# Kernel optimization log

Measured on AMD Instinct MI355X. Metric: run time of the kernel, lower is better.

## Reference

```python
import jax, jax.numpy as jnp
import numpy as np

D_MODEL = 1024
D_INTERNAL = 1024
B, T = 4, 2048
ROPE_BASE = 10000.0


def _rotate_half(x):
    h = x.shape[-1] // 2
    return jnp.concatenate([-x[..., h:], x[..., :h]], axis=-1)


def _justnorm(x):
    return x / jnp.linalg.norm(x, axis=-1, keepdims=True)


def setup_inputs() -> dict:
    key = jax.random.key(0)
    k1, k2 = jax.random.split(key)
    stdev = 1.0 / (D_MODEL + D_INTERNAL) ** 0.5
    qkv_w = jax.random.uniform(k1, (3 * D_INTERNAL, D_MODEL), minval=-stdev, maxval=stdev, dtype=jnp.float32)
    qkv_w = _justnorm(qkv_w)  # source normalizes qkv rows at init
    sqk = (D_MODEL ** -0.5) * jnp.ones((D_INTERNAL,), dtype=jnp.float32)  # sqk_init_scaling * ones
    input_vecs = jax.random.normal(k2, (B, T, D_MODEL), dtype=jnp.float32)
    return {"input_vecs": input_vecs, "qkv_w": qkv_w, "sqk": sqk}


def reference(input_vecs, qkv_w, sqk):
    d_model = input_vecs.shape[-1]
    d_int = qkv_w.shape[0] // 3
    t_len = input_vecs.shape[-2]

    # QKV projection: F.linear(x, W) == x @ W.T
    qkv = jnp.einsum('btc,dc->btd', input_vecs, qkv_w)
    Q, K, V = jnp.split(qkv, 3, axis=-1)  # each [B, T, d_int]

    # Rotary embeddings over full d_int
    inv_freq = 1.0 / (ROPE_BASE ** (jnp.arange(0, d_int, 2, dtype=jnp.float32) / d_int))
    t = jnp.arange(t_len, dtype=jnp.float32)
    freqs = t[:, None] * inv_freq[None, :]              # [T, d_int/2]
    emb = jnp.concatenate([freqs, freqs], axis=-1)      # [T, d_int]
    cos, sin = jnp.cos(emb), jnp.sin(emb)
    Q = Q * cos + _rotate_half(Q) * sin
    K = K * cos + _rotate_half(K) * sin

    # L2 QK-norm with learned per-channel scale (sqk * (1.0 / sqk_init_scaling))
    sqk_eff = sqk * (d_model ** 0.5)
    Q = _justnorm(Q) * sqk_eff
    K = _justnorm(K) * sqk_eff

    # SDPA, eval path: causal, dropout=0, scale = C ** 0.5
    scale = d_model ** 0.5
    scores = jnp.einsum('bqd,bkd->bqk', Q, K) * scale   # [B, T, T]
    causal = jnp.tril(jnp.ones((t_len, t_len), dtype=bool))
    scores = jnp.where(causal[None, :, :], scores, -jnp.inf)
    attn = jax.nn.softmax(scores, axis=-1)
    out = jnp.einsum('bqk,bkd->bqd', attn, V)
    return out
```

## Files before the change

### kernel.cpp

```cpp
#include <hip/hip_runtime.h>

typedef unsigned short u16;
typedef short s16x8 __attribute__((ext_vector_type(8)));
typedef float f32x4 __attribute__((ext_vector_type(4)));

__device__ __forceinline__ u16 f2bf(float f) {
    union { float f; unsigned u; } v; v.f = f;
    unsigned r = v.u + 0x7FFFu + ((v.u >> 16) & 1u);
    return (u16)(r >> 16);
}
__device__ __forceinline__ float bf2f(u16 h) {
    union { unsigned u; float f; } v; v.u = ((unsigned)h) << 16;
    return v.f;
}
__device__ __forceinline__ u16 f2h(float f) {
    _Float16 h = (_Float16)f;
    union { _Float16 h; u16 u; } v; v.h = h; return v.u;
}
__device__ __forceinline__ float h2f(u16 u) {
    union { u16 u; _Float16 h; } v; v.u = u; return (float)v.h;
}

__device__ __forceinline__ void gl_lds16(const u16* g, u16* l) {
    __builtin_amdgcn_global_load_lds(
        (const __attribute__((address_space(1))) void*)g,
        (__attribute__((address_space(3))) void*)l,
        16, 0, 0);
}

__global__ __launch_bounds__(256) void f32_to_bf16(const float* __restrict__ in,
                                                   u16* __restrict__ out, int n) {
    int i = (blockIdx.x * 256 + threadIdx.x) * 4;
    int stride = gridDim.x * 256 * 4;
    for (; i < n; i += stride) {
        float4 v = *reinterpret_cast<const float4*>(in + i);
        ushort4 o;
        o.x = f2bf(v.x); o.y = f2bf(v.y); o.z = f2bf(v.z); o.w = f2bf(v.w);
        *reinterpret_cast<ushort4*>(out + i) = o;
    }
}

template <typename CT>
__device__ __forceinline__ void store_c(CT* p, float v) {
    if constexpr (__is_same(CT, u16))            *p = f2bf(v);
    else if constexpr (__is_same(CT, _Float16))  *p = (_Float16)v;
    else                                         *p = v;
}

__device__ __forceinline__ s16x8 ldfrag(const u16* base, int row, int kk, int fq) {
    int cb = ((kk << 6) + (fq << 4)) ^ ((row & 7) << 4);
    return *reinterpret_cast<const s16x8*>(base + row * 64 + (cb >> 1));
}

template <int MODE, typename CT>
__global__ __launch_bounds__(512)
void gemm_bt(const u16* __restrict__ A, const u16* __restrict__ B, CT* __restrict__ C,
             int K, int lda, int ldb, int ldc, long sA, long sB, long sC) {
    int bx = blockIdx.x, by = blockIdx.y, bz = blockIdx.z;
    if (MODE == 0) {
        int bid = blockIdx.x;
        int xcd = bid & 7, idx = bid >> 3;
        int r = idx >> 6, w = idx & 63;
        bx = r * 8 + (w & 7);
        by = xcd * 8 + (w >> 3);
        bz = 0;
    }
    if (MODE == 1 && bx > by) return;
    if (MODE == 2) { bz = blockIdx.y & 3; by = 15 - (int)(blockIdx.y >> 2); }
    A += (size_t)bz * sA; B += (size_t)bz * sB; C += (size_t)bz * sC;
    int kend = K;
    if (MODE == 2) { int kl = (by + 1) * 128; kend = kl < K ? kl : K; }
    const int NT = kend >> 6;

    __shared__ u16 lds[32768];

    const int tid  = threadIdx.x;
    const int lane = tid & 63;
    const int wave = tid >> 6;
    const int wr = (wave >> 2) * 64;
    const int wc = (wave & 3) * 32;
    const int fr = lane & 15;
    const int fq = lane >> 4;
    const int tm = by * 128, tn = bx * 128;

    const int srow = tid >> 3;
    const int gco  = (((tid & 7) ^ (srow & 7)) << 3);
    const u16* aR[2]; const u16* bR[2];
#pragma unroll
    for (int j = 0; j < 2; ++j) {
        aR[j] = A + (size_t)(tm + j * 64 + srow) * lda + gco;
        bR[j] = B + (size_t)(tn + j * 64 + srow) * ldb + gco;
    }

#define STAGE(b2, k0) do {                                                        \
    _Pragma("unroll") for (int j = 0; j < 2; ++j)                                 \
        gl_lds16(aR[j] + (k0), lds + (b2) * 16384 + j * 4096 + wave * 512);       \
    _Pragma("unroll") for (int j = 0; j < 2; ++j)                                 \
        gl_lds16(bR[j] + (k0), lds + (b2) * 16384 + 8192 + j * 4096 + wave * 512);\
  } while (0)

    f32x4 acc[4][2];
#pragma unroll
    for (int m = 0; m < 4; ++m)
#pragma unroll
        for (int n = 0; n < 2; ++n) acc[m][n] = {0.f, 0.f, 0.f, 0.f};

    STAGE(0, 0);
    if (NT > 1) STAGE(1, 64);

    for (int t = 0; t < NT; ++t) {
        const int buf = t & 1;
        if (t + 1 < NT) { asm volatile("s_waitcnt vmcnt(4)" ::: "memory"); }
        else            { asm volatile("s_waitcnt vmcnt(0)" ::: "memory"); }
        __builtin_amdgcn_s_barrier();
        __builtin_amdgcn_sched_barrier(0);

        const u16* Ab = lds + buf * 16384;
        const u16* Bb = Ab + 8192;
        s16x8 bf0[2], bf1[2];
#pragma unroll
        for (int n = 0; n < 2; ++n) {
            bf0[n] = ldfrag(Bb, wc + n * 16 + fr, 0, fq);
            bf1[n] = ldfrag(Bb, wc + n * 16 + fr, 1, fq);
        }
        __builtin_amdgcn_s_setprio(1);
#pragma unroll
        for (int m = 0; m < 4; ++m) {
            s16x8 a0 = ldfrag(Ab, wr + m * 16 + fr, 0, fq);
            s16x8 a1 = ldfrag(Ab, wr + m * 16 + fr, 1, fq);
#pragma unroll
            for (int n = 0; n < 2; ++n) {
                acc[m][n] = __builtin_amdgcn_mfma_f32_16x16x32_bf16(a0, bf0[n], acc[m][n], 0, 0, 0);
                acc[m][n] = __builtin_amdgcn_mfma_f32_16x16x32_bf16(a1, bf1[n], acc[m][n], 0, 0, 0);
            }
        }
        __builtin_amdgcn_s_setprio(0);
        __builtin_amdgcn_sched_barrier(0);
        __builtin_amdgcn_s_barrier();
        if (t + 2 < NT) STAGE(buf, (t + 2) << 6);
    }
#undef STAGE

#pragma unroll
    for (int m = 0; m < 4; ++m)
#pragma unroll
        for (int n = 0; n < 2; ++n)
#pragma unroll
            for (int r = 0; r < 4; ++r) {
                int row = tm + wr + m * 16 + fq * 4 + r;
                int col = tn + wc + n * 16 + fr;
                store_c(&C[(size_t)row * ldc + col], acc[m][n][r]);
            }
}

__global__ __launch_bounds__(256)
void trig_table(u16* __restrict__ trig) {
    const int t = blockIdx.x;
    const float L = 0.025952563241307517f;
    u16* row = trig + (size_t)t * 1024;
#pragma unroll
    for (int i = 0; i < 2; ++i) {
        int d = threadIdx.x + i * 256;
        float invf = exp2f(-(float)d * L);
        float ang = (float)t * invf;
        float s, c;
        sincosf(ang, &s, &c);
        row[d] = f2h(c);
        row[512 + d] = f2h(s);
    }
}

__global__ __launch_bounds__(256)
void rope_norm(u16* __restrict__ qkv, const float* __restrict__ sqk,
               const u16* __restrict__ trig) {
    const int row = blockIdx.x;
    const int t = row & 2047;
    u16* qp = qkv + (size_t)row * 3072;
    u16* kp = qp + 1024;
    const u16* tb = trig + (size_t)t * 1024;
    const int d = threadIdx.x << 1;

    union U2 { uint u; u16 h[2]; };
    U2 qc0, qc1, kc0, kc1, cc, ss;
    qc0.u = *reinterpret_cast<const uint*>(qp + d);
    qc1.u = *reinterpret_cast<const uint*>(qp + 512 + d);
    kc0.u = *reinterpret_cast<const uint*>(kp + d);
    kc1.u = *reinterpret_cast<const uint*>(kp + 512 + d);
    cc.u  = *reinterpret_cast<const uint*>(tb + d);
    ss.u  = *reinterpret_cast<const uint*>(tb + 512 + d);

    float nq0[2], nq1[2], nk0[2], nk1[2];
    float ssq_q = 0.f, ssq_k = 0.f;
#pragma unroll
    for (int j = 0; j < 2; ++j) {
        float c = h2f(cc.h[j]), s = h2f(ss.h[j]);
        float q0 = bf2f(qc0.h[j]), q1 = bf2f(qc1.h[j]);
        float k0 = bf2f(kc0.h[j]), k1 = bf2f(kc1.h[j]);
        nq0[j] = q0 * c - q1 * s;
        nq1[j] = q1 * c + q0 * s;
        nk0[j] = k0 * c - k1 * s;
        nk1[j] = k1 * c + k0 * s;
        ssq_q += nq0[j] * nq0[j] + nq1[j] * nq1[j];
        ssq_k += nk0[j] * nk0[j] + nk1[j] * nk1[j];
    }

#pragma unroll
    for (int off = 32; off; off >>= 1) {
        ssq_q += __shfl_xor(ssq_q, off);
        ssq_k += __shfl_xor(ssq_k, off);
    }
    __shared__ float red[8];
    int wave = threadIdx.x >> 6, lane = threadIdx.x & 63;
    if (lane == 0) { red[wave] = ssq_q; red[4 + wave] = ssq_k; }
    __syncthreads();
    float rq = rsqrtf(red[0] + red[1] + red[2] + red[3]);
    float rk = rsqrtf(red[4] + red[5] + red[6] + red[7]);

    float2 sq0 = *reinterpret_cast<const float2*>(sqk + d);
    float2 sq1 = *reinterpret_cast<const float2*>(sqk + 512 + d);
    float s0[2] = {sq0.x * 32.f, sq0.y * 32.f};
    float s1[2] = {sq1.x * 32.f, sq1.y * 32.f};

    U2 oq0, oq1, ok0, ok1;
#pragma unroll
    for (int j = 0; j < 2; ++j) {
        oq0.h[j] = f2bf(nq0[j] * rq * s0[j]);
        oq1.h[j] = f2bf(nq1[j] * rq * s1[j]);
        ok0.h[j] = f2bf(nk0[j] * rk * s0[j]);
        ok1.h[j] = f2bf(nk1[j] * rk * s1[j]);
    }
    *reinterpret_cast<uint*>(qp + d)       = oq0.u;
    *reinterpret_cast<uint*>(qp + 512 + d) = oq1.u;
    *reinterpret_cast<uint*>(kp + d)       = ok0.u;
    *reinterpret_cast<uint*>(kp + 512 + d) = ok1.u;
}

__global__ __launch_bounds__(256)
void transpose_v(const u16* __restrict__ qkv, u16* __restrict__ VT) {
    __shared__ u16 tile[32][33];
    int b = blockIdx.z;
    int n0 = blockIdx.x * 32;
    int k0 = blockIdx.y * 32;
    int tx = threadIdx.x, ty = threadIdx.y;
    const u16* src = qkv + (size_t)b * 2048 * 3072 + 2048;
#pragma unroll
    for (int i = 0; i < 4; ++i)
        tile[ty + i * 8][tx] = src[(size_t)(k0 + ty + i * 8) * 3072 + n0 + tx];
    __syncthreads();
    u16* dst = VT + (size_t)b * 1024 * 2048;
#pragma unroll
    for (int i = 0; i < 4; ++i)
        dst[(size_t)(n0 + ty + i * 8) * 2048 + k0 + tx] = tile[tx][ty + i * 8];
}

__global__ __launch_bounds__(256)
void softmax_inplace(u16* __restrict__ Sbase) {
    const int r = blockIdx.x;
    const int b = blockIdx.y;
    u16* row = Sbase + (size_t)b * 4194304 + (size_t)r * 2048;
    const int n = r + 1;
    const int kcap = ((r >> 7) + 1) << 7;
    const int tid = threadIdx.x;
    const bool act = (tid * 8) < kcap;

    union { uint4 u; u16 h[8]; } U;
    if (act) U.u = *reinterpret_cast<const uint4*>(row + tid * 8);
    float v[8];
    float m = -1e30f;
#pragma unroll
    for (int i = 0; i < 8; ++i) {
        int c = tid * 8 + i;
        v[i] = (act && c < n) ? h2f(U.h[i]) : -1e30f;
        m = fmaxf(m, v[i]);
    }
#pragma unroll
    for (int off = 32; off; off >>= 1) m = fmaxf(m, __shfl_xor(m, off));
    __shared__ float redm[4], redsum[4];
    int wave = tid >> 6, lane = tid & 63;
    if (lane == 0) redm[wave] = m;
    __syncthreads();
    m = fmaxf(fmaxf(redm[0], redm[1]), fmaxf(redm[2], redm[3]));
    float M = 32.f * m;

    float sum = 0.f;
#pragma unroll
    for (int i = 0; i < 8; ++i) {
        int c = tid * 8 + i;
        float e = (v[i] > -1e29f) ? __expf(32.f * v[i] - M) : 0.f;
        if (c >= n) e = 0.f;
        v[i] = e;
        sum += e;
    }
#pragma unroll
    for (int off = 32; off; off >>= 1) sum += __shfl_xor(sum, off);
    if (lane == 0) redsum[wave] = sum;
    __syncthreads();
    sum = redsum[0] + redsum[1] + redsum[2] + redsum[3];
    float inv = 1.f / sum;

    if (act) {
        union { uint4 u; u16 h[8]; } O;
#pragma unroll
        for (int i = 0; i < 8; ++i) O.h[i] = f2bf(v[i] * inv);
        *reinterpret_cast<uint4*>(row + tid * 8) = O.u;
    }
}

extern "C" void kernel_launch(void* const* d_in, const int* in_sizes, int n_in,
                              void* d_out, int out_size, void* d_ws, size_t ws_size,
                              hipStream_t stream) {
    const float* x   = (const float*)d_in[0];
    const float* w   = (const float*)d_in[1];
    const float* sqk = (const float*)d_in[2];
    float* out = (float*)d_out;

    const size_t SZ_XB  = (size_t)8192 * 1024 * 2;
    const size_t SZ_WB  = (size_t)3072 * 1024 * 2;
    const size_t SZ_QKV = (size_t)8192 * 3072 * 2;
    const size_t SZ_S   = (size_t)4 * 2048 * 2048 * 2;
    const size_t SZ_TR  = (size_t)2048 * 1024 * 2;
    if (ws_size < SZ_XB + SZ_WB + SZ_QKV + SZ_S + SZ_TR) return;

    char* ws = (char*)d_ws;
    u16* xb   = (u16*)ws;  ws += SZ_XB;
    u16* wb   = (u16*)ws;  ws += SZ_WB;
    u16* qkv  = (u16*)ws;  ws += SZ_QKV;
    u16* S    = (u16*)ws;  ws += SZ_S;
    u16* trig = (u16*)ws;
    u16* VT   = xb;

    f32_to_bf16<<<2048, 256, 0, stream>>>(x, xb, 8192 * 1024);
    f32_to_bf16<<<768, 256, 0, stream>>>(w, wb, 3072 * 1024);

    gemm_bt<0, u16><<<dim3(1536, 1, 1), 512, 0, stream>>>(
        xb, wb, qkv, 1024, 1024, 1024, 3072, 0, 0, 0);

    trig_table<<<2048, 256, 0, stream>>>(trig);
    rope_norm<<<8192, 256, 0, stream>>>(qkv, sqk, trig);

    transpose_v<<<dim3(32, 64, 4), dim3(32, 8), 0, stream>>>(qkv, VT);

    gemm_bt<1, _Float16><<<dim3(16, 16, 4), 512, 0, stream>>>(
        qkv, qkv + 1024, (_Float16*)S, 1024, 3072, 3072, 2048,
        (long)2048 * 3072, (long)2048 * 3072, (long)2048 * 2048);

    softmax_inplace<<<dim3(2048, 4), 256, 0, stream>>>(S);

    gemm_bt<2, float><<<dim3(8, 64, 1), 512, 0, stream>>>(
        S, VT, out, 2048, 2048, 2048, 1024,
        (long)2048 * 2048, (long)1024 * 2048, (long)2048 * 1024);
}
```

Baseline: 167.4 us.

## Enlarge GEMM tiles to 256 rows and fuse V transpose into QKV GEMM epilogue

```diff
diff --git a/kernel.cpp b/kernel.cpp
--- a/kernel.cpp
+++ b/kernel.cpp
@@ -52,84 +52,94 @@
     return *reinterpret_cast<const s16x8*>(base + row * 64 + (cb >> 1));
 }
 
-template <int MODE, typename CT>
-__global__ __launch_bounds__(512)
+template <int MODE, int BNT, typename CT>
+__global__ __launch_bounds__(512, 2)
 void gemm_bt(const u16* __restrict__ A, const u16* __restrict__ B, CT* __restrict__ C,
+             u16* __restrict__ VT,
              int K, int lda, int ldb, int ldc, long sA, long sB, long sC) {
-    int bx = blockIdx.x, by = blockIdx.y, bz = blockIdx.z;
+    constexpr int NF = BNT / 64;
+    constexpr int SB = 16384 + BNT * 64;
+
+    int bx, by, bz;
     if (MODE == 0) {
         int bid = blockIdx.x;
         int xcd = bid & 7, idx = bid >> 3;
-        int r = idx >> 6, w = idx & 63;
-        bx = r * 8 + (w & 7);
-        by = xcd * 8 + (w >> 3);
+        bx = idx % 12;
+        by = xcd * 4 + idx / 12;
         bz = 0;
+    } else {
+        bx = blockIdx.x; by = blockIdx.y; bz = blockIdx.z;
     }
     if (MODE == 1 && bx > by) return;
-    if (MODE == 2) { bz = blockIdx.y & 3; by = 15 - (int)(blockIdx.y >> 2); }
+    if (MODE == 2) by = 7 - by;
     A += (size_t)bz * sA; B += (size_t)bz * sB; C += (size_t)bz * sC;
     int kend = K;
-    if (MODE == 2) { int kl = (by + 1) * 128; kend = kl < K ? kl : K; }
+    if (MODE == 2) { int kl = (by + 1) * 256; kend = kl < K ? kl : K; }
     const int NT = kend >> 6;
 
-    __shared__ u16 lds[32768];
+    __shared__ u16 lds[2 * SB];
 
     const int tid  = threadIdx.x;
     const int lane = tid & 63;
     const int wave = tid >> 6;
-    const int wr = (wave >> 2) * 64;
-    const int wc = (wave & 3) * 32;
+    const int wr = (wave >> 2) * 128;
+    const int wc = (wave & 3) * (BNT / 4);
     const int fr = lane & 15;
     const int fq = lane >> 4;
-    const int tm = by * 128, tn = bx * 128;
+    const int tm = by * 256, tn = bx * BNT;
 
     const int srow = tid >> 3;
     const int gco  = (((tid & 7) ^ (srow & 7)) << 3);
-    const u16* aR[2]; const u16* bR[2];
-#pragma unroll
-    for (int j = 0; j < 2; ++j) {
+    const u16* aR[4]; const u16* bR[NF];
+#pragma unroll
+    for (int j = 0; j < 4; ++j)
         aR[j] = A + (size_t)(tm + j * 64 + srow) * lda + gco;
+#pragma unroll
+    for (int j = 0; j < NF; ++j)
         bR[j] = B + (size_t)(tn + j * 64 + srow) * ldb + gco;
-    }
 
 #define STAGE(b2, k0) do {                                                        \
-    _Pragma("unroll") for (int j = 0; j < 2; ++j)                                 \
-        gl_lds16(aR[j] + (k0), lds + (b2) * 16384 + j * 4096 + wave * 512);       \
-    _Pragma("unroll") for (int j = 0; j < 2; ++j)                                 \
-        gl_lds16(bR[j] + (k0), lds + (b2) * 16384 + 8192 + j * 4096 + wave * 512);\
+    _Pragma("unroll") for (int j = 0; j < 4; ++j)                                 \
+        gl_lds16(aR[j] + (k0), lds + (b2) * SB + j * 4096 + wave * 512);          \
+    _Pragma("unroll") for (int j = 0; j < NF; ++j)                                \
+        gl_lds16(bR[j] + (k0), lds + (b2) * SB + 16384 + j * 4096 + wave * 512);  \
   } while (0)
 
-    f32x4 acc[4][2];
-#pragma unroll
-    for (int m = 0; m < 4; ++m)
-#pragma unroll
-        for (int n = 0; n < 2; ++n) acc[m][n] = {0.f, 0.f, 0.f, 0.f};
+    f32x4 acc[8][NF];
+#pragma unroll
+    for (int m = 0; m < 8; ++m)
+#pragma unroll
+        for (int n = 0; n < NF; ++n) acc[m][n] = {0.f, 0.f, 0.f, 0.f};
 
     STAGE(0, 0);
     if (NT > 1) STAGE(1, 64);
 
     for (int t = 0; t < NT; ++t) {
         const int buf = t & 1;
-        if (t + 1 < NT) { asm volatile("s_waitcnt vmcnt(4)" ::: "memory"); }
-        else            { asm volatile("s_waitcnt vmcnt(0)" ::: "memory"); }
+        if (t + 1 < NT) {
+            if constexpr (NF == 4) asm volatile("s_waitcnt vmcnt(8)" ::: "memory");
+            else                   asm volatile("s_waitcnt vmcnt(6)" ::: "memory");
+        } else {
+            asm volatile("s_waitcnt vmcnt(0)" ::: "memory");
+        }
         __builtin_amdgcn_s_barrier();
         __builtin_amdgcn_sched_barrier(0);
 
-        const u16* Ab = lds + buf * 16384;
-        const u16* Bb = Ab + 8192;
-        s16x8 bf0[2], bf1[2];
-#pragma unroll
-        for (int n = 0; n < 2; ++n) {
+        const u16* Ab = lds + buf * SB;
+        const u16* Bb = Ab + 16384;
+        s16x8 bf0[NF], bf1[NF];
+#pragma unroll
+        for (int n = 0; n < NF; ++n) {
             bf0[n] = ldfrag(Bb, wc + n * 16 + fr, 0, fq);
             bf1[n] = ldfrag(Bb, wc + n * 16 + fr, 1, fq);
         }
         __builtin_amdgcn_s_setprio(1);
 #pragma unroll
-        for (int m = 0; m < 4; ++m) {
+        for (int m = 0; m < 8; ++m) {
             s16x8 a0 = ldfrag(Ab, wr + m * 16 + fr, 0, fq);
             s16x8 a1 = ldfrag(Ab, wr + m * 16 + fr, 1, fq);
 #pragma unroll
-            for (int n = 0; n < 2; ++n) {
+            for (int n = 0; n < NF; ++n) {
                 acc[m][n] = __builtin_amdgcn_mfma_f32_16x16x32_bf16(a0, bf0[n], acc[m][n], 0, 0, 0);
                 acc[m][n] = __builtin_amdgcn_mfma_f32_16x16x32_bf16(a1, bf1[n], acc[m][n], 0, 0, 0);
             }
@@ -141,16 +151,30 @@
     }
 #undef STAGE
 
-#pragma unroll
-    for (int m = 0; m < 4; ++m)
-#pragma unroll
-        for (int n = 0; n < 2; ++n)
-#pragma unroll
-            for (int r = 0; r < 4; ++r) {
-                int row = tm + wr + m * 16 + fq * 4 + r;
-                int col = tn + wc + n * 16 + fr;
-                store_c(&C[(size_t)row * ldc + col], acc[m][n][r]);
-            }
+    if (MODE == 0 && tn >= 2048) {
+#pragma unroll
+        for (int m = 0; m < 8; ++m)
+#pragma unroll
+            for (int n = 0; n < NF; ++n)
+#pragma unroll
+                for (int r = 0; r < 4; ++r) {
+                    int row = tm + wr + m * 16 + fq * 4 + r;
+                    int col = tn + wc + n * 16 + fr;
+                    VT[((size_t)(row >> 11)) * 2097152 + (size_t)(col - 2048) * 2048 + (row & 2047)]
+                        = f2bf(acc[m][n][r]);
+                }
+    } else {
+#pragma unroll
+        for (int m = 0; m < 8; ++m)
+#pragma unroll
+            for (int n = 0; n < NF; ++n)
+#pragma unroll
+                for (int r = 0; r < 4; ++r) {
+                    int row = tm + wr + m * 16 + fq * 4 + r;
+                    int col = tn + wc + n * 16 + fr;
+                    store_c(&C[(size_t)row * ldc + col], acc[m][n][r]);
+                }
+    }
 }
 
 __global__ __launch_bounds__(256)
@@ -171,11 +195,11 @@
 }
 
 __global__ __launch_bounds__(256)
-void rope_norm(u16* __restrict__ qkv, const float* __restrict__ sqk,
+void rope_norm(u16* __restrict__ qk, const float* __restrict__ sqk,
                const u16* __restrict__ trig) {
     const int row = blockIdx.x;
     const int t = row & 2047;
-    u16* qp = qkv + (size_t)row * 3072;
+    u16* qp = qk + (size_t)row * 2048;
     u16* kp = qp + 1024;
     const u16* tb = trig + (size_t)t * 1024;
     const int d = threadIdx.x << 1;
@@ -236,30 +260,12 @@
 }
 
 __global__ __launch_bounds__(256)
-void transpose_v(const u16* __restrict__ qkv, u16* __restrict__ VT) {
-    __shared__ u16 tile[32][33];
-    int b = blockIdx.z;
-    int n0 = blockIdx.x * 32;
-    int k0 = blockIdx.y * 32;
-    int tx = threadIdx.x, ty = threadIdx.y;
-    const u16* src = qkv + (size_t)b * 2048 * 3072 + 2048;
-#pragma unroll
-    for (int i = 0; i < 4; ++i)
-        tile[ty + i * 8][tx] = src[(size_t)(k0 + ty + i * 8) * 3072 + n0 + tx];
-    __syncthreads();
-    u16* dst = VT + (size_t)b * 1024 * 2048;
-#pragma unroll
-    for (int i = 0; i < 4; ++i)
-        dst[(size_t)(n0 + ty + i * 8) * 2048 + k0 + tx] = tile[tx][ty + i * 8];
-}
-
-__global__ __launch_bounds__(256)
 void softmax_inplace(u16* __restrict__ Sbase) {
     const int r = blockIdx.x;
     const int b = blockIdx.y;
     u16* row = Sbase + (size_t)b * 4194304 + (size_t)r * 2048;
     const int n = r + 1;
-    const int kcap = ((r >> 7) + 1) << 7;
+    const int kcap = ((r >> 8) + 1) << 8;
     const int tid = threadIdx.x;
     const bool act = (tid * 8) < kcap;
 
@@ -316,37 +322,36 @@
 
     const size_t SZ_XB  = (size_t)8192 * 1024 * 2;
     const size_t SZ_WB  = (size_t)3072 * 1024 * 2;
-    const size_t SZ_QKV = (size_t)8192 * 3072 * 2;
+    const size_t SZ_QK  = (size_t)8192 * 2048 * 2;
+    const size_t SZ_VT  = (size_t)4 * 1024 * 2048 * 2;
     const size_t SZ_S   = (size_t)4 * 2048 * 2048 * 2;
     const size_t SZ_TR  = (size_t)2048 * 1024 * 2;
-    if (ws_size < SZ_XB + SZ_WB + SZ_QKV + SZ_S + SZ_TR) return;
+    if (ws_size < SZ_XB + SZ_WB + SZ_QK + SZ_VT + SZ_S + SZ_TR) return;
 
     char* ws = (char*)d_ws;
     u16* xb   = (u16*)ws;  ws += SZ_XB;
     u16* wb   = (u16*)ws;  ws += SZ_WB;
-    u16* qkv  = (u16*)ws;  ws += SZ_QKV;
+    u16* qk   = (u16*)ws;  ws += SZ_QK;
+    u16* VT   = (u16*)ws;  ws += SZ_VT;
     u16* S    = (u16*)ws;  ws += SZ_S;
     u16* trig = (u16*)ws;
-    u16* VT   = xb;
 
     f32_to_bf16<<<2048, 256, 0, stream>>>(x, xb, 8192 * 1024);
     f32_to_bf16<<<768, 256, 0, stream>>>(w, wb, 3072 * 1024);
-
-    gemm_bt<0, u16><<<dim3(1536, 1, 1), 512, 0, stream>>>(
-        xb, wb, qkv, 1024, 1024, 1024, 3072, 0, 0, 0);
-
     trig_table<<<2048, 256, 0, stream>>>(trig);
-    rope_norm<<<8192, 256, 0, stream>>>(qkv, sqk, trig);
-
-    transpose_v<<<dim3(32, 64, 4), dim3(32, 8), 0, stream>>>(qkv, VT);
-
-    gemm_bt<1, _Float16><<<dim3(16, 16, 4), 512, 0, stream>>>(
-        qkv, qkv + 1024, (_Float16*)S, 1024, 3072, 3072, 2048,
-        (long)2048 * 3072, (long)2048 * 3072, (long)2048 * 2048);
+
+    gemm_bt<0, 256, u16><<<dim3(384, 1, 1), 512, 0, stream>>>(
+        xb, wb, qk, VT, 1024, 1024, 1024, 2048, 0, 0, 0);
+
+    rope_norm<<<8192, 256, 0, stream>>>(qk, sqk, trig);
+
+    gemm_bt<1, 256, _Float16><<<dim3(8, 8, 4), 512, 0, stream>>>(
+        qk, qk + 1024, (_Float16*)S, nullptr, 1024, 2048, 2048, 2048,
+        (long)2048 * 2048, (long)2048 * 2048, (long)2048 * 2048);
 
     softmax_inplace<<<dim3(2048, 4), 256, 0, stream>>>(S);
 
-    gemm_bt<2, float><<<dim3(8, 64, 1), 512, 0, stream>>>(
-        S, VT, out, 2048, 2048, 2048, 1024,
+    gemm_bt<2, 128, float><<<dim3(8, 8, 4), 512, 0, stream>>>(
+        S, VT, out, nullptr, 2048, 2048, 2048, 1024,
         (long)2048 * 2048, (long)1024 * 2048, (long)2048 * 1024);
 }
```

New measurement: 188.5 us. +12.6%, slower.

## Fuse V transpose into a larger-tile QKV GEMM epilogue

Applied to the files above, without the earlier changes.

```diff
diff --git a/kernel.cpp b/kernel.cpp
--- a/kernel.cpp
+++ b/kernel.cpp
@@ -52,19 +52,133 @@
     return *reinterpret_cast<const s16x8*>(base + row * 64 + (cb >> 1));
 }
 
+#define MFMA16(a, b, c) __builtin_amdgcn_mfma_f32_16x16x32_bf16((a), (b), (c), 0, 0, 0)
+
+__global__ __launch_bounds__(512, 1)
+void qkv_gemm(const u16* __restrict__ A, const u16* __restrict__ B,
+              u16* __restrict__ qk, u16* __restrict__ VT, int lda, int ldb) {
+    const int bid = blockIdx.x;
+    const int xcd = bid & 7, idx = bid >> 3;
+    const int bx = idx % 12;
+    const int by = xcd * 4 + idx / 12;
+    const int NT = 16;
+
+    __shared__ u16 lds[65536];
+
+    const int tid  = threadIdx.x;
+    const int lane = tid & 63;
+    const int wave = tid >> 6;
+    const int wr = (wave >> 2) * 128;
+    const int wc = (wave & 3) * 64;
+    const int fr = lane & 15;
+    const int fq = lane >> 4;
+    const int tm = by * 256, tn = bx * 256;
+
+    const int srow = tid >> 3;
+    const int gco  = (((tid & 7) ^ (srow & 7)) << 3);
+    const u16* gA[4]; const u16* gB[4];
+#pragma unroll
+    for (int j = 0; j < 4; ++j) {
+        gA[j] = A + (size_t)(tm + j * 64 + srow) * lda + gco;
+        gB[j] = B + (size_t)(tn + j * 64 + srow) * ldb + gco;
+    }
+
+#define STA(s_, j_, k_) gl_lds16(gA[j_] + (k_), lds + (s_) * 32768 + (j_) * 4096 + wave * 512)
+#define STB(s_, j_, k_) gl_lds16(gB[j_] + (k_), lds + (s_) * 32768 + 16384 + (j_) * 4096 + wave * 512)
+
+    f32x4 acc[8][4];
+#pragma unroll
+    for (int m = 0; m < 8; ++m)
+#pragma unroll
+        for (int n = 0; n < 4; ++n) acc[m][n] = {0.f, 0.f, 0.f, 0.f};
+
+    STB(0, 0, 0); STB(0, 1, 0); STB(0, 2, 0); STB(0, 3, 0);
+    STA(0, 0, 0); STA(0, 1, 0); STA(0, 2, 0); STA(0, 3, 0);
+
+#define PHASE_REST(p)                                                         \
+  {                                                                           \
+    if (t + 1 < NT) {                                                         \
+      if ((p) == 1) { STB(ns, 2, nk); STB(ns, 3, nk); }                       \
+      if ((p) == 2) { STA(ns, 0, nk); STA(ns, 1, nk); }                       \
+      if ((p) == 3) { STA(ns, 2, nk); STA(ns, 3, nk); }                       \
+    }                                                                         \
+    s16x8 a0 = ldfrag(Ab, wr + (2 * (p)) * 16 + fr, 0, fq);                   \
+    s16x8 a1 = ldfrag(Ab, wr + (2 * (p)) * 16 + fr, 1, fq);                   \
+    s16x8 a2 = ldfrag(Ab, wr + (2 * (p) + 1) * 16 + fr, 0, fq);               \
+    s16x8 a3 = ldfrag(Ab, wr + (2 * (p) + 1) * 16 + fr, 1, fq);               \
+    asm volatile("s_waitcnt lgkmcnt(0)" ::: "memory");                        \
+    __builtin_amdgcn_sched_barrier(0);                                        \
+    __builtin_amdgcn_s_setprio(1);                                            \
+    _Pragma("unroll") for (int n = 0; n < 4; ++n) {                           \
+      acc[2 * (p)][n]     = MFMA16(a0, bf0[n], acc[2 * (p)][n]);              \
+      acc[2 * (p)][n]     = MFMA16(a1, bf1[n], acc[2 * (p)][n]);              \
+      acc[2 * (p) + 1][n] = MFMA16(a2, bf0[n], acc[2 * (p) + 1][n]);          \
+      acc[2 * (p) + 1][n] = MFMA16(a3, bf1[n], acc[2 * (p) + 1][n]);          \
+    }                                                                         \
+    __builtin_amdgcn_s_setprio(0);                                            \
+    __builtin_amdgcn_sched_barrier(0);                                        \
+  }
+
+    for (int t = 0; t < NT; ++t) {
+        const int s = t & 1, ns = s ^ 1, nk = (t + 1) << 6;
+        const u16* Ab = lds + s * 32768;
+        const u16* Bb = Ab + 16384;
+        s16x8 bf0[4], bf1[4];
+
+        if (t + 1 < NT) {
+            STB(ns, 0, nk); STB(ns, 1, nk);
+            asm volatile("s_waitcnt vmcnt(2)" ::: "memory");
+        } else {
+            asm volatile("s_waitcnt vmcnt(0)" ::: "memory");
+        }
+        __builtin_amdgcn_s_barrier();
+        __builtin_amdgcn_sched_barrier(0);
+#pragma unroll
+        for (int n = 0; n < 4; ++n) {
+            bf0[n] = ldfrag(Bb, wc + n * 16 + fr, 0, fq);
+            bf1[n] = ldfrag(Bb, wc + n * 16 + fr, 1, fq);
+        }
+        PHASE_REST(0)
+        PHASE_REST(1)
+        PHASE_REST(2)
+        PHASE_REST(3)
+        __builtin_amdgcn_s_barrier();
+    }
+#undef PHASE_REST
+#undef STA
+#undef STB
+
+    if (tn >= 2048) {
+#pragma unroll
+        for (int m = 0; m < 8; ++m)
+#pragma unroll
+            for (int n = 0; n < 4; ++n)
+#pragma unroll
+                for (int r = 0; r < 4; ++r) {
+                    int row = tm + wr + m * 16 + fq * 4 + r;
+                    int col = tn + wc + n * 16 + fr;
+                    VT[((size_t)(row >> 11)) * 2097152 + (size_t)(col - 2048) * 2048 + (row & 2047)]
+                        = f2bf(acc[m][n][r]);
+                }
+    } else {
+#pragma unroll
+        for (int m = 0; m < 8; ++m)
+#pragma unroll
+            for (int n = 0; n < 4; ++n)
+#pragma unroll
+                for (int r = 0; r < 4; ++r) {
+                    int row = tm + wr + m * 16 + fq * 4 + r;
+                    int col = tn + wc + n * 16 + fr;
+                    qk[(size_t)row * 2048 + col] = f2bf(acc[m][n][r]);
+                }
+    }
+}
+
 template <int MODE, typename CT>
 __global__ __launch_bounds__(512)
 void gemm_bt(const u16* __restrict__ A, const u16* __restrict__ B, CT* __restrict__ C,
              int K, int lda, int ldb, int ldc, long sA, long sB, long sC) {
     int bx = blockIdx.x, by = blockIdx.y, bz = blockIdx.z;
-    if (MODE == 0) {
-        int bid = blockIdx.x;
-        int xcd = bid & 7, idx = bid >> 3;
-        int r = idx >> 6, w = idx & 63;
-        bx = r * 8 + (w & 7);
-        by = xcd * 8 + (w >> 3);
-        bz = 0;
-    }
     if (MODE == 1 && bx > by) return;
     if (MODE == 2) { bz = blockIdx.y & 3; by = 15 - (int)(blockIdx.y >> 2); }
     A += (size_t)bz * sA; B += (size_t)bz * sB; C += (size_t)bz * sC;
@@ -130,8 +244,8 @@
             s16x8 a1 = ldfrag(Ab, wr + m * 16 + fr, 1, fq);
 #pragma unroll
             for (int n = 0; n < 2; ++n) {
-                acc[m][n] = __builtin_amdgcn_mfma_f32_16x16x32_bf16(a0, bf0[n], acc[m][n], 0, 0, 0);
-                acc[m][n] = __builtin_amdgcn_mfma_f32_16x16x32_bf16(a1, bf1[n], acc[m][n], 0, 0, 0);
+                acc[m][n] = MFMA16(a0, bf0[n], acc[m][n]);
+                acc[m][n] = MFMA16(a1, bf1[n], acc[m][n]);
             }
         }
         __builtin_amdgcn_s_setprio(0);
@@ -171,11 +285,11 @@
 }
 
 __global__ __launch_bounds__(256)
-void rope_norm(u16* __restrict__ qkv, const float* __restrict__ sqk,
+void rope_norm(u16* __restrict__ qk, const float* __restrict__ sqk,
                const u16* __restrict__ trig) {
     const int row = blockIdx.x;
     const int t = row & 2047;
-    u16* qp = qkv + (size_t)row * 3072;
+    u16* qp = qk + (size_t)row * 2048;
     u16* kp = qp + 1024;
     const u16* tb = trig + (size_t)t * 1024;
     const int d = threadIdx.x << 1;
@@ -236,24 +350,6 @@
 }
 
 __global__ __launch_bounds__(256)
-void transpose_v(const u16* __restrict__ qkv, u16* __restrict__ VT) {
-    __shared__ u16 tile[32][33];
-    int b = blockIdx.z;
-    int n0 = blockIdx.x * 32;
-    int k0 = blockIdx.y * 32;
-    int tx = threadIdx.x, ty = threadIdx.y;
-    const u16* src = qkv + (size_t)b * 2048 * 3072 + 2048;
-#pragma unroll
-    for (int i = 0; i < 4; ++i)
-        tile[ty + i * 8][tx] = src[(size_t)(k0 + ty + i * 8) * 3072 + n0 + tx];
-    __syncthreads();
-    u16* dst = VT + (size_t)b * 1024 * 2048;
-#pragma unroll
-    for (int i = 0; i < 4; ++i)
-        dst[(size_t)(n0 + ty + i * 8) * 2048 + k0 + tx] = tile[tx][ty + i * 8];
-}
-
-__global__ __launch_bounds__(256)
 void softmax_inplace(u16* __restrict__ Sbase) {
     const int r = blockIdx.x;
     const int b = blockIdx.y;
@@ -316,33 +412,31 @@
 
     const size_t SZ_XB  = (size_t)8192 * 1024 * 2;
     const size_t SZ_WB  = (size_t)3072 * 1024 * 2;
-    const size_t SZ_QKV = (size_t)8192 * 3072 * 2;
+    const size_t SZ_QK  = (size_t)8192 * 2048 * 2;
+    const size_t SZ_VT  = (size_t)4 * 1024 * 2048 * 2;
     const size_t SZ_S   = (size_t)4 * 2048 * 2048 * 2;
     const size_t SZ_TR  = (size_t)2048 * 1024 * 2;
-    if (ws_size < SZ_XB + SZ_WB + SZ_QKV + SZ_S + SZ_TR) return;
+    if (ws_size < SZ_XB + SZ_WB + SZ_QK + SZ_VT + SZ_S + SZ_TR) return;
 
     char* ws = (char*)d_ws;
     u16* xb   = (u16*)ws;  ws += SZ_XB;
     u16* wb   = (u16*)ws;  ws += SZ_WB;
-    u16* qkv  = (u16*)ws;  ws += SZ_QKV;
+    u16* qk   = (u16*)ws;  ws += SZ_QK;
+    u16* VT   = (u16*)ws;  ws += SZ_VT;
     u16* S    = (u16*)ws;  ws += SZ_S;
     u16* trig = (u16*)ws;
-    u16* VT   = xb;
 
     f32_to_bf16<<<2048, 256, 0, stream>>>(x, xb, 8192 * 1024);
     f32_to_bf16<<<768, 256, 0, stream>>>(w, wb, 3072 * 1024);
-
-    gemm_bt<0, u16><<<dim3(1536, 1, 1), 512, 0, stream>>>(
-        xb, wb, qkv, 1024, 1024, 1024, 3072, 0, 0, 0);
-
     trig_table<<<2048, 256, 0, stream>>>(trig);
-    rope_norm<<<8192, 256, 0, stream>>>(qkv, sqk, trig);
-
-    transpose_v<<<dim3(32, 64, 4), dim3(32, 8), 0, stream>>>(qkv, VT);
+
+    qkv_gemm<<<dim3(384, 1, 1), 512, 0, stream>>>(xb, wb, qk, VT, 1024, 1024);
+
+    rope_norm<<<8192, 256, 0, stream>>>(qk, sqk, trig);
 
     gemm_bt<1, _Float16><<<dim3(16, 16, 4), 512, 0, stream>>>(
-        qkv, qkv + 1024, (_Float16*)S, 1024, 3072, 3072, 2048,
-        (long)2048 * 3072, (long)2048 * 3072, (long)2048 * 2048);
+        qk, qk + 1024, (_Float16*)S, 1024, 2048, 2048, 2048,
+        (long)2048 * 2048, (long)2048 * 2048, (long)2048 * 2048);
 
     softmax_inplace<<<dim3(2048, 4), 256, 0, stream>>>(S);
 
```

Result: no change. 167.6 us (+0.2%).

## Fuse V transpose into QKV GEMM epilogue and merge prep kernels

Applied to the files above, without the earlier changes.

```diff
diff --git a/kernel.cpp b/kernel.cpp
--- a/kernel.cpp
+++ b/kernel.cpp
@@ -28,18 +28,6 @@
         16, 0, 0);
 }
 
-__global__ __launch_bounds__(256) void f32_to_bf16(const float* __restrict__ in,
-                                                   u16* __restrict__ out, int n) {
-    int i = (blockIdx.x * 256 + threadIdx.x) * 4;
-    int stride = gridDim.x * 256 * 4;
-    for (; i < n; i += stride) {
-        float4 v = *reinterpret_cast<const float4*>(in + i);
-        ushort4 o;
-        o.x = f2bf(v.x); o.y = f2bf(v.y); o.z = f2bf(v.z); o.w = f2bf(v.w);
-        *reinterpret_cast<ushort4*>(out + i) = o;
-    }
-}
-
 template <typename CT>
 __device__ __forceinline__ void store_c(CT* p, float v) {
     if constexpr (__is_same(CT, u16))            *p = f2bf(v);
@@ -52,18 +40,62 @@
     return *reinterpret_cast<const s16x8*>(base + row * 64 + (cb >> 1));
 }
 
+#define MFMA16(a, b, c) __builtin_amdgcn_mfma_f32_16x16x32_bf16((a), (b), (c), 0, 0, 0)
+
+__global__ __launch_bounds__(256)
+void prep(const float* __restrict__ x, const float* __restrict__ w,
+          u16* __restrict__ xb, u16* __restrict__ wb, u16* __restrict__ trig) {
+    const int bid = blockIdx.x;
+    if (bid < 2048) {
+        int i = (bid * 256 + threadIdx.x) * 4;
+        const int stride = 2048 * 256 * 4;
+        for (; i < 8192 * 1024; i += stride) {
+            float4 v = *reinterpret_cast<const float4*>(x + i);
+            ushort4 o;
+            o.x = f2bf(v.x); o.y = f2bf(v.y); o.z = f2bf(v.z); o.w = f2bf(v.w);
+            *reinterpret_cast<ushort4*>(xb + i) = o;
+        }
+    } else if (bid < 2816) {
+        int i = ((bid - 2048) * 256 + threadIdx.x) * 4;
+        const int stride = 768 * 256 * 4;
+        for (; i < 3072 * 1024; i += stride) {
+            float4 v = *reinterpret_cast<const float4*>(w + i);
+            ushort4 o;
+            o.x = f2bf(v.x); o.y = f2bf(v.y); o.z = f2bf(v.z); o.w = f2bf(v.w);
+            *reinterpret_cast<ushort4*>(wb + i) = o;
+        }
+    } else {
+        const int t = bid - 2816;
+        const float L = 0.025952563241307517f;
+        u16* row = trig + (size_t)t * 1024;
+#pragma unroll
+        for (int i = 0; i < 2; ++i) {
+            int d = threadIdx.x + i * 256;
+            float invf = exp2f(-(float)d * L);
+            float ang = (float)t * invf;
+            float s, c;
+            sincosf(ang, &s, &c);
+            row[d] = f2h(c);
+            row[512 + d] = f2h(s);
+        }
+    }
+}
+
 template <int MODE, typename CT>
 __global__ __launch_bounds__(512)
 void gemm_bt(const u16* __restrict__ A, const u16* __restrict__ B, CT* __restrict__ C,
+             u16* __restrict__ VT,
              int K, int lda, int ldb, int ldc, long sA, long sB, long sC) {
-    int bx = blockIdx.x, by = blockIdx.y, bz = blockIdx.z;
+    int bx, by, bz;
     if (MODE == 0) {
         int bid = blockIdx.x;
         int xcd = bid & 7, idx = bid >> 3;
-        int r = idx >> 6, w = idx & 63;
-        bx = r * 8 + (w & 7);
-        by = xcd * 8 + (w >> 3);
+        int r = idx >> 6, w2 = idx & 63;
+        bx = r * 8 + (w2 & 7);
+        by = xcd * 8 + (w2 >> 3);
         bz = 0;
+    } else {
+        bx = blockIdx.x; by = blockIdx.y; bz = blockIdx.z;
     }
     if (MODE == 1 && bx > by) return;
     if (MODE == 2) { bz = blockIdx.y & 3; by = 15 - (int)(blockIdx.y >> 2); }
@@ -130,8 +162,8 @@
             s16x8 a1 = ldfrag(Ab, wr + m * 16 + fr, 1, fq);
 #pragma unroll
             for (int n = 0; n < 2; ++n) {
-                acc[m][n] = __builtin_amdgcn_mfma_f32_16x16x32_bf16(a0, bf0[n], acc[m][n], 0, 0, 0);
-                acc[m][n] = __builtin_amdgcn_mfma_f32_16x16x32_bf16(a1, bf1[n], acc[m][n], 0, 0, 0);
+                acc[m][n] = MFMA16(a0, bf0[n], acc[m][n]);
+                acc[m][n] = MFMA16(a1, bf1[n], acc[m][n]);
             }
         }
         __builtin_amdgcn_s_setprio(0);
@@ -141,41 +173,38 @@
     }
 #undef STAGE
 
-#pragma unroll
-    for (int m = 0; m < 4; ++m)
-#pragma unroll
-        for (int n = 0; n < 2; ++n)
-#pragma unroll
-            for (int r = 0; r < 4; ++r) {
-                int row = tm + wr + m * 16 + fq * 4 + r;
-                int col = tn + wc + n * 16 + fr;
-                store_c(&C[(size_t)row * ldc + col], acc[m][n][r]);
-            }
+    if (MODE == 0 && tn >= 2048) {
+#pragma unroll
+        for (int m = 0; m < 4; ++m)
+#pragma unroll
+            for (int n = 0; n < 2; ++n)
+#pragma unroll
+                for (int r = 0; r < 4; ++r) {
+                    int row = tm + wr + m * 16 + fq * 4 + r;
+                    int col = tn + wc + n * 16 + fr;
+                    VT[((size_t)(row >> 11)) * 2097152 + (size_t)(col - 2048) * 2048 + (row & 2047)]
+                        = f2bf(acc[m][n][r]);
+                }
+    } else {
+#pragma unroll
+        for (int m = 0; m < 4; ++m)
+#pragma unroll
+            for (int n = 0; n < 2; ++n)
+#pragma unroll
+                for (int r = 0; r < 4; ++r) {
+                    int row = tm + wr + m * 16 + fq * 4 + r;
+                    int col = tn + wc + n * 16 + fr;
+                    store_c(&C[(size_t)row * ldc + col], acc[m][n][r]);
+                }
+    }
 }
 
 __global__ __launch_bounds__(256)
-void trig_table(u16* __restrict__ trig) {
-    const int t = blockIdx.x;
-    const float L = 0.025952563241307517f;
-    u16* row = trig + (size_t)t * 1024;
-#pragma unroll
-    for (int i = 0; i < 2; ++i) {
-        int d = threadIdx.x + i * 256;
-        float invf = exp2f(-(float)d * L);
-        float ang = (float)t * invf;
-        float s, c;
-        sincosf(ang, &s, &c);
-        row[d] = f2h(c);
-        row[512 + d] = f2h(s);
-    }
-}
-
-__global__ __launch_bounds__(256)
-void rope_norm(u16* __restrict__ qkv, const float* __restrict__ sqk,
+void rope_norm(u16* __restrict__ qk, const float* __restrict__ sqk,
                const u16* __restrict__ trig) {
     const int row = blockIdx.x;
     const int t = row & 2047;
-    u16* qp = qkv + (size_t)row * 3072;
+    u16* qp = qk + (size_t)row * 2048;
     u16* kp = qp + 1024;
     const u16* tb = trig + (size_t)t * 1024;
     const int d = threadIdx.x << 1;
@@ -236,24 +265,6 @@
 }
 
 __global__ __launch_bounds__(256)
-void transpose_v(const u16* __restrict__ qkv, u16* __restrict__ VT) {
-    __shared__ u16 tile[32][33];
-    int b = blockIdx.z;
-    int n0 = blockIdx.x * 32;
-    int k0 = blockIdx.y * 32;
-    int tx = threadIdx.x, ty = threadIdx.y;
-    const u16* src = qkv + (size_t)b * 2048 * 3072 + 2048;
-#pragma unroll
-    for (int i = 0; i < 4; ++i)
-        tile[ty + i * 8][tx] = src[(size_t)(k0 + ty + i * 8) * 3072 + n0 + tx];
-    __syncthreads();
-    u16* dst = VT + (size_t)b * 1024 * 2048;
-#pragma unroll
-    for (int i = 0; i < 4; ++i)
-        dst[(size_t)(n0 + ty + i * 8) * 2048 + k0 + tx] = tile[tx][ty + i * 8];
-}
-
-__global__ __launch_bounds__(256)
 void softmax_inplace(u16* __restrict__ Sbase) {
     const int r = blockIdx.x;
     const int b = blockIdx.y;
@@ -316,37 +327,34 @@
 
     const size_t SZ_XB  = (size_t)8192 * 1024 * 2;
     const size_t SZ_WB  = (size_t)3072 * 1024 * 2;
-    const size_t SZ_QKV = (size_t)8192 * 3072 * 2;
+    const size_t SZ_QK  = (size_t)8192 * 2048 * 2;
+    const size_t SZ_VT  = (size_t)4 * 1024 * 2048 * 2;
     const size_t SZ_S   = (size_t)4 * 2048 * 2048 * 2;
     const size_t SZ_TR  = (size_t)2048 * 1024 * 2;
-    if (ws_size < SZ_XB + SZ_WB + SZ_QKV + SZ_S + SZ_TR) return;
+    if (ws_size < SZ_XB + SZ_WB + SZ_QK + SZ_VT + SZ_S + SZ_TR) return;
 
     char* ws = (char*)d_ws;
     u16* xb   = (u16*)ws;  ws += SZ_XB;
     u16* wb   = (u16*)ws;  ws += SZ_WB;
-    u16* qkv  = (u16*)ws;  ws += SZ_QKV;
+    u16* qk   = (u16*)ws;  ws += SZ_QK;
+    u16* VT   = (u16*)ws;  ws += SZ_VT;
     u16* S    = (u16*)ws;  ws += SZ_S;
     u16* trig = (u16*)ws;
-    u16* VT   = xb;
-
-    f32_to_bf16<<<2048, 256, 0, stream>>>(x, xb, 8192 * 1024);
-    f32_to_bf16<<<768, 256, 0, stream>>>(w, wb, 3072 * 1024);
+
+    prep<<<4864, 256, 0, stream>>>(x, w, xb, wb, trig);
 
     gemm_bt<0, u16><<<dim3(1536, 1, 1), 512, 0, stream>>>(
-        xb, wb, qkv, 1024, 1024, 1024, 3072, 0, 0, 0);
-
-    trig_table<<<2048, 256, 0, stream>>>(trig);
-    rope_norm<<<8192, 256, 0, stream>>>(qkv, sqk, trig);
-
-    transpose_v<<<dim3(32, 64, 4), dim3(32, 8), 0, stream>>>(qkv, VT);
+        xb, wb, qk, VT, 1024, 1024, 1024, 2048, 0, 0, 0);
+
+    rope_norm<<<8192, 256, 0, stream>>>(qk, sqk, trig);
 
     gemm_bt<1, _Float16><<<dim3(16, 16, 4), 512, 0, stream>>>(
-        qkv, qkv + 1024, (_Float16*)S, 1024, 3072, 3072, 2048,
-        (long)2048 * 3072, (long)2048 * 3072, (long)2048 * 2048);
+        qk, qk + 1024, (_Float16*)S, nullptr, 1024, 2048, 2048, 2048,
+        (long)2048 * 2048, (long)2048 * 2048, (long)2048 * 2048);
 
     softmax_inplace<<<dim3(2048, 4), 256, 0, stream>>>(S);
 
     gemm_bt<2, float><<<dim3(8, 64, 1), 512, 0, stream>>>(
-        S, VT, out, 2048, 2048, 2048, 1024,
+        S, VT, out, nullptr, 2048, 2048, 2048, 1024,
         (long)2048 * 2048, (long)1024 * 2048, (long)2048 * 1024);
 }
```

New measurement: 157.1 us. -6.1%, faster.
